# Optimization experiments

Measured on AMD Instinct MI355X. Metric: run time of the kernel, lower is better.

The kernel has to match this reference:

```python
import jax, jax.numpy as jnp
import numpy as np

C = 1000      # num_classes
U = 10        # proxies_per_class
D = 512       # feature_dim
B = 4096      # batch
ALPHA = 32.0
DELTA = 0.1


def _l2norm(x, axis=-1):
    return x / jnp.linalg.norm(x, axis=axis, keepdims=True).clip(1e-12)


def setup_inputs() -> dict:
    key = jax.random.key(0)
    k1, k2, k3 = jax.random.split(key, 3)
    features = jax.random.normal(k1, (B, D), dtype=jnp.float32)
    labels = jax.random.randint(k2, (B,), 0, C)
    # proxies are initialized to row-normalized gaussians (as in __init__)
    proxies = _l2norm(jax.random.normal(k3, (C * U, D), dtype=jnp.float32))
    return {"features": features, "labels": labels, "proxies": proxies}


def reference(features, labels, proxies):
    # proxy_class_ids: [C*U], class id of each proxy
    class_ids = jnp.repeat(jnp.arange(C), U)

    x = _l2norm(features)          # [B, D]
    p = _l2norm(proxies)           # [P, D], P = C*U
    sim = x @ p.T                  # [B, P]

    # ---- infer_logits, agg='soft', tau=1 ----
    s = sim.reshape(B, C, U)       # per-class proxy similarities
    w = jax.nn.softmax(s, axis=2)
    logits = jnp.sum(w * s, axis=2)  # [B, C], tau=1 so no extra scaling

    # ---- _compute_proxy_loss (Proxy-Anchor) ----
    sim_t = sim.T                                         # [P, B]
    pos_mask = labels[None, :] == class_ids[:, None]      # [P, B]
    neg_inf = jnp.finfo(jnp.float32).min
    z_pos = jnp.where(pos_mask, -ALPHA * (sim_t - DELTA), neg_inf)
    z_neg = jnp.where(pos_mask, neg_inf, ALPHA * (sim_t + DELTA))
    lse_pos = jax.nn.logsumexp(z_pos, axis=1)             # [P]
    lse_neg = jax.nn.logsumexp(z_neg, axis=1)             # [P]
    pos_term = jax.nn.softplus(lse_pos)
    neg_term = jax.nn.softplus(lse_neg)
    has_pos = pos_mask.any(axis=1)
    pos_loss = jnp.where(has_pos, pos_term, 0.0).sum() / jnp.maximum(
        has_pos.sum(), 1).astype(jnp.float32)
    neg_loss = neg_term.mean()
    proxy_loss = pos_loss + neg_loss

    return logits, proxy_loss
```

## Files before the change

### kernel.cpp

```cpp
#include <hip/hip_runtime.h>
#include <hip/hip_bf16.h>

#define C_CLS   1000
#define U_PX    10
#define D_DIM   512
#define B_BATCH 4096
#define P_PX    (C_CLS * U_PX)
#define ALPHA_F 32.0f
#define DELTA_F 0.1f

#define BM 128
#define BN 80
#define BK 64
#define SIMP 84

#define A_OFF   0
#define B_OFF   16384
#define SMEM_SZ 26624

#define ZERO_DBL (2 * P_PX + 4)
#define FIN_BLK  ((P_PX + 255) / 256)

typedef __attribute__((ext_vector_type(8))) short bf16x8;
typedef __attribute__((ext_vector_type(4))) float f32x4;

typedef __attribute__((address_space(1))) const void gv_t;
typedef __attribute__((address_space(3))) void lv_t;

__device__ __forceinline__ void gload_lds16(const void* g, void* lds) {
    __builtin_amdgcn_global_load_lds((gv_t*)g, (lv_t*)lds, 16, 0, 0);
}

__device__ __forceinline__ unsigned int f2bf(float f) {
    union { float f; unsigned u; } c; c.f = f;
    unsigned u = c.u;
    return (u + 0x7FFF + ((u >> 16) & 1)) >> 16;
}

__global__ __launch_bounds__(256) void norm_rows_kernel(const float* __restrict__ feat,
                                                        const float* __restrict__ prox,
                                                        unsigned int* __restrict__ xout,
                                                        unsigned int* __restrict__ pout,
                                                        double* __restrict__ zbase) {
    const int zidx = blockIdx.x * 256 + threadIdx.x;
    if (zidx < ZERO_DBL) zbase[zidx] = 0.0;

    const int wid  = threadIdx.x >> 6;
    const int lane = threadIdx.x & 63;
    int row = blockIdx.x * 4 + wid;
    const float* in;
    unsigned int* out;
    if (row < B_BATCH) { in = feat + (size_t)row * D_DIM;   out = xout + (size_t)row * (D_DIM / 2); }
    else { row -= B_BATCH; in = prox + (size_t)row * D_DIM; out = pout + (size_t)row * (D_DIM / 2); }
    const float4 v0 = reinterpret_cast<const float4*>(in)[lane * 2];
    const float4 v1 = reinterpret_cast<const float4*>(in)[lane * 2 + 1];
    float ss = v0.x*v0.x + v0.y*v0.y + v0.z*v0.z + v0.w*v0.w
             + v1.x*v1.x + v1.y*v1.y + v1.z*v1.z + v1.w*v1.w;
    #pragma unroll
    for (int off = 1; off < 64; off <<= 1) ss += __shfl_xor(ss, off, 64);
    const float inv = 1.0f / fmaxf(sqrtf(ss), 1e-12f);
    uint4 o;
    o.x = f2bf(v0.x * inv) | (f2bf(v0.y * inv) << 16);
    o.y = f2bf(v0.z * inv) | (f2bf(v0.w * inv) << 16);
    o.z = f2bf(v1.x * inv) | (f2bf(v1.y * inv) << 16);
    o.w = f2bf(v1.z * inv) | (f2bf(v1.w * inv) << 16);
    *reinterpret_cast<uint4*>(out + lane * 4) = o;
}

__global__ __launch_bounds__(256, 4) void fused_gemm_kernel(
    const unsigned short* __restrict__ xbf,
    const unsigned short* __restrict__ pbf,
    const int*            __restrict__ labels,
    float*                __restrict__ logits,
    double*               __restrict__ pos_sum,
    double*               __restrict__ neg_sum)
{
    __shared__ __align__(16) char smem[SMEM_SZ];
    __shared__ int lab_lds[BM];

    const int t    = threadIdx.x;
    const int m0   = blockIdx.x * BM;
    const int n0   = blockIdx.y * BN;
    const int wid  = t >> 6;
    const int lane = t & 63;
    const int l15  = lane & 15;
    const int kgrp = lane >> 4;

    if (t < BM) lab_lds[t] = labels[m0 + t];

    const int srow = lane >> 3;
    const int scol = (lane & 7) ^ srow;

    const int koff0 = ((kgrp    ) ^ (l15 & 7)) << 4;
    const int koff1 = ((kgrp + 4) ^ (l15 & 7)) << 4;

    f32x4 acc[2][5];
    #pragma unroll
    for (int m = 0; m < 2; ++m)
        #pragma unroll
        for (int n = 0; n < 5; ++n) acc[m][n] = (f32x4){0.f, 0.f, 0.f, 0.f};

    for (int ks = 0; ks < D_DIM / BK; ++ks) {
        const int kbase = ks * BK;
        #pragma unroll
        for (int c = wid; c < 16; c += 4)
            gload_lds16(xbf + (size_t)(m0 + c * 8 + srow) * D_DIM + kbase + scol * 8,
                        smem + A_OFF + c * 1024);
        for (int c = wid; c < 10; c += 4)
            gload_lds16(pbf + (size_t)(n0 + c * 8 + srow) * D_DIM + kbase + scol * 8,
                        smem + B_OFF + c * 1024);
        __syncthreads();
        __builtin_amdgcn_s_setprio(1);
        #pragma unroll
        for (int kk8 = 0; kk8 < 2; ++kk8) {
            const int koff = kk8 ? koff1 : koff0;
            bf16x8 b[5];
            #pragma unroll
            for (int n = 0; n < 5; ++n)
                b[n] = *reinterpret_cast<const bf16x8*>(smem + B_OFF + (n * 16 + l15) * 128 + koff);
            #pragma unroll
            for (int m = 0; m < 2; ++m) {
                const bf16x8 a = *reinterpret_cast<const bf16x8*>(
                    smem + A_OFF + (wid * 32 + m * 16 + l15) * 128 + koff);
                #pragma unroll
                for (int n = 0; n < 5; ++n)
                    acc[m][n] = __builtin_amdgcn_mfma_f32_16x16x32_bf16(a, b[n], acc[m][n], 0, 0, 0);
            }
        }
        __builtin_amdgcn_s_setprio(0);
        __syncthreads();
    }

    {
        int labv[8];
        #pragma unroll
        for (int m = 0; m < 2; ++m)
            #pragma unroll
            for (int r = 0; r < 4; ++r)
                labv[m * 4 + r] = lab_lds[wid * 32 + m * 16 + kgrp * 4 + r];
        #pragma unroll
        for (int n = 0; n < 5; ++n) {
            const int col = n * 16 + l15;
            const int cls = (n0 + col) / U_PX;
            float pos = 0.f, neg = 0.f;
            #pragma unroll
            for (int m = 0; m < 2; ++m)
                #pragma unroll
                for (int r = 0; r < 4; ++r) {
                    const float s = acc[m][n][r];
                    const bool isp = (labv[m * 4 + r] == cls);
                    const float e = __expf(isp ? (-ALPHA_F * (s - DELTA_F))
                                               : ( ALPHA_F * (s + DELTA_F)));
                    if (isp) pos += e; else neg += e;
                }
            pos += __shfl_xor(pos, 16, 64); pos += __shfl_xor(pos, 32, 64);
            neg += __shfl_xor(neg, 16, 64); neg += __shfl_xor(neg, 32, 64);
            if (lane < 16) {
                atomicAdd(&neg_sum[n0 + col], (double)neg);
                if (pos != 0.f) atomicAdd(&pos_sum[n0 + col], (double)pos);
            }
        }
    }

    float* simw = reinterpret_cast<float*>(smem) + wid * (16 * SIMP);
    #pragma unroll
    for (int m = 0; m < 2; ++m) {
        #pragma unroll
        for (int n = 0; n < 5; ++n)
            #pragma unroll
            for (int r = 0; r < 4; ++r)
                simw[(kgrp * 4 + r) * SIMP + n * 16 + l15] = acc[m][n][r];
        #pragma unroll
        for (int it = 0; it < 2; ++it) {
            const int j   = lane + it * 64;
            const int r   = j >> 3;
            const int c   = j & 7;
            const float* s = simw + r * SIMP + c * U_PX;
            float wsum = 0.f, wssum = 0.f;
            #pragma unroll
            for (int u = 0; u < U_PX; ++u) {
                const float sv = s[u];
                const float e = __expf(sv);
                wsum += e; wssum += e * sv;
            }
            logits[(size_t)(m0 + wid * 32 + m * 16 + r) * C_CLS + (n0 / U_PX + c)] = wssum / wsum;
        }
        __builtin_amdgcn_s_waitcnt(0);
    }
}

__global__ __launch_bounds__(256) void finalize_kernel(
    const double* __restrict__ pos_sum,
    const double* __restrict__ neg_sum,
    double*       __restrict__ accum,
    float*        __restrict__ out_loss)
{
    const int p = blockIdx.x * 256 + threadIdx.x;
    double pv = 0.0, nv = 0.0;
    int c = 0;
    if (p < P_PX) {
        nv = log1p(neg_sum[p]);
        const double ps = pos_sum[p];
        if (ps != 0.0) { pv = log1p(ps); c = 1; }
    }
    #pragma unroll
    for (int off = 1; off < 64; off <<= 1) {
        pv += __shfl_xor(pv, off, 64);
        nv += __shfl_xor(nv, off, 64);
        c  += __shfl_xor(c,  off, 64);
    }
    if ((threadIdx.x & 63) == 0) {
        atomicAdd(&accum[0], pv);
        atomicAdd(&accum[1], nv);
        atomicAdd((int*)(accum + 2), c);
    }
    __syncthreads();
    __threadfence();
    if (threadIdx.x == 0) {
        const unsigned prev = atomicAdd((unsigned*)(accum + 3), 1u);
        if (prev == FIN_BLK - 1) {
            const double a0 = atomicAdd(&accum[0], 0.0);
            const double a1 = atomicAdd(&accum[1], 0.0);
            const int   cnt = atomicAdd((int*)(accum + 2), 0);
            out_loss[0] = (float)(a0 / (double)max(cnt, 1) + a1 / (double)P_PX);
        }
    }
}

extern "C" void kernel_launch(void* const* d_in, const int* in_sizes, int n_in,
                              void* d_out, int out_size, void* d_ws, size_t ws_size,
                              hipStream_t stream) {
    const float* features = (const float*)d_in[0];
    const int*   labels   = (const int*)d_in[1];
    const float* proxies  = (const float*)d_in[2];
    float* out = (float*)d_out;

    char* ws = (char*)d_ws;
    unsigned short* xbf = (unsigned short*)ws;
    unsigned short* pbf = (unsigned short*)(ws + (size_t)B_BATCH * D_DIM * 2);
    double* pos_sum = (double*)(ws + (size_t)(B_BATCH + P_PX) * D_DIM * 2);
    double* neg_sum = pos_sum + P_PX;
    double* accum   = neg_sum + P_PX;

    norm_rows_kernel<<<(B_BATCH + P_PX) / 4, 256, 0, stream>>>(
        features, proxies, (unsigned int*)xbf, (unsigned int*)pbf, pos_sum);

    fused_gemm_kernel<<<dim3(B_BATCH / BM, P_PX / BN), 256, 0, stream>>>(
        xbf, pbf, labels, out, pos_sum, neg_sum);

    finalize_kernel<<<FIN_BLK, 256, 0, stream>>>(pos_sum, neg_sum, accum,
                                                 out + (size_t)B_BATCH * C_CLS);
}
```

Baseline: 93.96 us.

## Keep full A row-panel resident in LDS and loop persistently over proxy tiles

Each block now loads its whole 128x512 feature panel into LDS once (128KB) and loops over 16 proxy tiles in a persistent grid of 256 blocks, instead of reloading A per output tile. Proxy tiles are double-buffered so the next K slice is fetched while MFMAs run. The aim is to cut redundant global/L2 traffic for A and per-block launch/prologue costs. In exchange, the large LDS footprint limits occupancy to one block per CU, and the grid of 256 blocks may leave load-balance tails.

```diff
diff --git a/kernel.cpp b/kernel.cpp
--- a/kernel.cpp
+++ b/kernel.cpp
@@ -12,11 +12,14 @@
 #define BM 128
 #define BN 80
 #define BK 64
-#define SIMP 84
-
-#define A_OFF   0
-#define B_OFF   16384
-#define SMEM_SZ 26624
+#define NKS (D_DIM / BK)
+#define NNT (P_PX / BN)
+#define SIMP 80
+
+#define A_OFF    0
+#define B_OFF    131072
+#define B_STRIDE 10240
+#define SMEM_SZ  (131072 + 2 * B_STRIDE)
 
 #define ZERO_DBL (2 * P_PX + 4)
 #define FIN_BLK  ((P_PX + 255) / 256)
@@ -67,7 +70,7 @@
     *reinterpret_cast<uint4*>(out + lane * 4) = o;
 }
 
-__global__ __launch_bounds__(256, 4) void fused_gemm_kernel(
+__global__ __launch_bounds__(256) void fused_gemm_kernel(
     const unsigned short* __restrict__ xbf,
     const unsigned short* __restrict__ pbf,
     const int*            __restrict__ labels,
@@ -79,8 +82,10 @@
     __shared__ int lab_lds[BM];
 
     const int t    = threadIdx.x;
-    const int m0   = blockIdx.x * BM;
-    const int n0   = blockIdx.y * BN;
+    const int bx   = blockIdx.x;
+    const int mi   = bx >> 3;
+    const int nr   = bx & 7;
+    const int m0   = mi * BM;
     const int wid  = t >> 6;
     const int lane = t & 63;
     const int l15  = lane & 15;
@@ -88,105 +93,136 @@
 
     if (t < BM) lab_lds[t] = labels[m0 + t];
 
-    const int srow = lane >> 3;
-    const int scol = (lane & 7) ^ srow;
-
+    const int srow  = lane >> 3;
+    const int scolB = (lane & 7) ^ srow;
     const int koff0 = ((kgrp    ) ^ (l15 & 7)) << 4;
     const int koff1 = ((kgrp + 4) ^ (l15 & 7)) << 4;
 
+    for (int c = wid; c < BM; c += 4) {
+        const int gc = lane ^ (c & 7);
+        gload_lds16(xbf + (size_t)(m0 + c) * D_DIM + gc * 8,
+                    smem + A_OFF + c * 1024);
+    }
+    {
+        const int n0f = nr * BN;
+        for (int c = wid; c < 10; c += 4)
+            gload_lds16(pbf + (size_t)(n0f + c * 8 + srow) * D_DIM + scolB * 8,
+                        smem + B_OFF + c * 1024);
+    }
+    asm volatile("s_waitcnt vmcnt(0)\n\ts_barrier" ::: "memory");
+
     f32x4 acc[2][5];
-    #pragma unroll
-    for (int m = 0; m < 2; ++m)
-        #pragma unroll
-        for (int n = 0; n < 5; ++n) acc[m][n] = (f32x4){0.f, 0.f, 0.f, 0.f};
-
-    for (int ks = 0; ks < D_DIM / BK; ++ks) {
-        const int kbase = ks * BK;
-        #pragma unroll
-        for (int c = wid; c < 16; c += 4)
-            gload_lds16(xbf + (size_t)(m0 + c * 8 + srow) * D_DIM + kbase + scol * 8,
-                        smem + A_OFF + c * 1024);
-        for (int c = wid; c < 10; c += 4)
-            gload_lds16(pbf + (size_t)(n0 + c * 8 + srow) * D_DIM + kbase + scol * 8,
-                        smem + B_OFF + c * 1024);
-        __syncthreads();
-        __builtin_amdgcn_s_setprio(1);
-        #pragma unroll
-        for (int kk8 = 0; kk8 < 2; ++kk8) {
-            const int koff = kk8 ? koff1 : koff0;
-            bf16x8 b[5];
-            #pragma unroll
-            for (int n = 0; n < 5; ++n)
-                b[n] = *reinterpret_cast<const bf16x8*>(smem + B_OFF + (n * 16 + l15) * 128 + koff);
-            #pragma unroll
-            for (int m = 0; m < 2; ++m) {
-                const bf16x8 a = *reinterpret_cast<const bf16x8*>(
-                    smem + A_OFF + (wid * 32 + m * 16 + l15) * 128 + koff);
-                #pragma unroll
-                for (int n = 0; n < 5; ++n)
-                    acc[m][n] = __builtin_amdgcn_mfma_f32_16x16x32_bf16(a, b[n], acc[m][n], 0, 0, 0);
-            }
-        }
-        __builtin_amdgcn_s_setprio(0);
-        __syncthreads();
-    }
-
-    {
-        int labv[8];
+
+    #define STAGE_B(n0_, ks_, buf_)                                                     \
+        do {                                                                            \
+            for (int c_ = wid; c_ < 10; c_ += 4)                                        \
+                gload_lds16(pbf + (size_t)((n0_) + c_ * 8 + srow) * D_DIM               \
+                                + (ks_) * BK + scolB * 8,                               \
+                            smem + B_OFF + (buf_) * B_STRIDE + c_ * 1024);              \
+        } while (0)
+
+    for (int jt = nr; jt < NNT; jt += 8) {
+        const int n0 = jt * BN;
         #pragma unroll
         for (int m = 0; m < 2; ++m)
             #pragma unroll
-            for (int r = 0; r < 4; ++r)
-                labv[m * 4 + r] = lab_lds[wid * 32 + m * 16 + kgrp * 4 + r];
+            for (int n = 0; n < 5; ++n) acc[m][n] = (f32x4){0.f, 0.f, 0.f, 0.f};
+
+        for (int ks = 0; ks < NKS; ++ks) {
+            const int cur = ks & 1;
+            if (ks < NKS - 1) STAGE_B(n0, ks + 1, cur ^ 1);
+            __builtin_amdgcn_sched_barrier(0);
+            __builtin_amdgcn_s_setprio(1);
+            #pragma unroll
+            for (int kk8 = 0; kk8 < 2; ++kk8) {
+                const int koff = kk8 ? koff1 : koff0;
+                bf16x8 b[5];
+                #pragma unroll
+                for (int n = 0; n < 5; ++n)
+                    b[n] = *reinterpret_cast<const bf16x8*>(
+                        smem + B_OFF + cur * B_STRIDE + (n * 16 + l15) * 128 + koff);
+                const int kch = ks * 8 + kk8 * 4 + kgrp;
+                const int aoff = ((kch ^ (l15 & 7)) << 4);
+                #pragma unroll
+                for (int m = 0; m < 2; ++m) {
+                    const bf16x8 a = *reinterpret_cast<const bf16x8*>(
+                        smem + A_OFF + (wid * 32 + m * 16 + l15) * 1024 + aoff);
+                    #pragma unroll
+                    for (int n = 0; n < 5; ++n)
+                        acc[m][n] = __builtin_amdgcn_mfma_f32_16x16x32_bf16(
+                            a, b[n], acc[m][n], 0, 0, 0);
+                }
+            }
+            __builtin_amdgcn_s_setprio(0);
+            asm volatile("s_waitcnt lgkmcnt(0)" ::: "memory");
+            __builtin_amdgcn_sched_barrier(0);
+            asm volatile("s_waitcnt vmcnt(0)\n\ts_barrier" ::: "memory");
+        }
+
+        {
+            int labv[8];
+            #pragma unroll
+            for (int m = 0; m < 2; ++m)
+                #pragma unroll
+                for (int r = 0; r < 4; ++r)
+                    labv[m * 4 + r] = lab_lds[wid * 32 + m * 16 + kgrp * 4 + r];
+            #pragma unroll
+            for (int n = 0; n < 5; ++n) {
+                const int col = n * 16 + l15;
+                const int cls = (n0 + col) / U_PX;
+                float pos = 0.f, neg = 0.f;
+                #pragma unroll
+                for (int m = 0; m < 2; ++m)
+                    #pragma unroll
+                    for (int r = 0; r < 4; ++r) {
+                        const float s = acc[m][n][r];
+                        const bool isp = (labv[m * 4 + r] == cls);
+                        const float e = __expf(isp ? (-ALPHA_F * (s - DELTA_F))
+                                                   : ( ALPHA_F * (s + DELTA_F)));
+                        if (isp) pos += e; else neg += e;
+                    }
+                pos += __shfl_xor(pos, 16, 64); pos += __shfl_xor(pos, 32, 64);
+                neg += __shfl_xor(neg, 16, 64); neg += __shfl_xor(neg, 32, 64);
+                if (lane < 16) {
+                    atomicAdd(&neg_sum[n0 + col], (double)neg);
+                    if (pos != 0.f) atomicAdd(&pos_sum[n0 + col], (double)pos);
+                }
+            }
+        }
+
+        float* simw = reinterpret_cast<float*>(smem + B_OFF) + wid * (16 * SIMP);
         #pragma unroll
-        for (int n = 0; n < 5; ++n) {
-            const int col = n * 16 + l15;
-            const int cls = (n0 + col) / U_PX;
-            float pos = 0.f, neg = 0.f;
-            #pragma unroll
-            for (int m = 0; m < 2; ++m)
-                #pragma unroll
-                for (int r = 0; r < 4; ++r) {
-                    const float s = acc[m][n][r];
-                    const bool isp = (labv[m * 4 + r] == cls);
-                    const float e = __expf(isp ? (-ALPHA_F * (s - DELTA_F))
-                                               : ( ALPHA_F * (s + DELTA_F)));
-                    if (isp) pos += e; else neg += e;
+        for (int m = 0; m < 2; ++m) {
+            #pragma unroll
+            for (int n = 0; n < 5; ++n)
+                #pragma unroll
+                for (int r = 0; r < 4; ++r)
+                    simw[(kgrp * 4 + r) * SIMP + n * 16 + l15] = acc[m][n][r];
+            #pragma unroll
+            for (int it = 0; it < 2; ++it) {
+                const int j = lane + it * 64;
+                const int r = j >> 3;
+                const int c = j & 7;
+                const float* s = simw + r * SIMP + c * U_PX;
+                float wsum = 0.f, wssum = 0.f;
+                #pragma unroll
+                for (int u = 0; u < U_PX; ++u) {
+                    const float sv = s[u];
+                    const float e = __expf(sv);
+                    wsum += e; wssum += e * sv;
                 }
-            pos += __shfl_xor(pos, 16, 64); pos += __shfl_xor(pos, 32, 64);
-            neg += __shfl_xor(neg, 16, 64); neg += __shfl_xor(neg, 32, 64);
-            if (lane < 16) {
-                atomicAdd(&neg_sum[n0 + col], (double)neg);
-                if (pos != 0.f) atomicAdd(&pos_sum[n0 + col], (double)pos);
+                logits[(size_t)(m0 + wid * 32 + m * 16 + r) * C_CLS + (jt * 8 + c)] = wssum / wsum;
             }
-        }
-    }
-
-    float* simw = reinterpret_cast<float*>(smem) + wid * (16 * SIMP);
-    #pragma unroll
-    for (int m = 0; m < 2; ++m) {
-        #pragma unroll
-        for (int n = 0; n < 5; ++n)
-            #pragma unroll
-            for (int r = 0; r < 4; ++r)
-                simw[(kgrp * 4 + r) * SIMP + n * 16 + l15] = acc[m][n][r];
-        #pragma unroll
-        for (int it = 0; it < 2; ++it) {
-            const int j   = lane + it * 64;
-            const int r   = j >> 3;
-            const int c   = j & 7;
-            const float* s = simw + r * SIMP + c * U_PX;
-            float wsum = 0.f, wssum = 0.f;
-            #pragma unroll
-            for (int u = 0; u < U_PX; ++u) {
-                const float sv = s[u];
-                const float e = __expf(sv);
-                wsum += e; wssum += e * sv;
-            }
-            logits[(size_t)(m0 + wid * 32 + m * 16 + r) * C_CLS + (n0 / U_PX + c)] = wssum / wsum;
-        }
-        __builtin_amdgcn_s_waitcnt(0);
-    }
+            __builtin_amdgcn_s_waitcnt(0);
+        }
+
+        __builtin_amdgcn_s_barrier();
+        if (jt + 8 < NNT) {
+            STAGE_B((jt + 8) * BN, 0, 0);
+            asm volatile("s_waitcnt vmcnt(0)\n\ts_barrier" ::: "memory");
+        }
+    }
+    #undef STAGE_B
 }
 
 __global__ __launch_bounds__(256) void finalize_kernel(
@@ -245,7 +281,7 @@
     norm_rows_kernel<<<(B_BATCH + P_PX) / 4, 256, 0, stream>>>(
         features, proxies, (unsigned int*)xbf, (unsigned int*)pbf, pos_sum);
 
-    fused_gemm_kernel<<<dim3(B_BATCH / BM, P_PX / BN), 256, 0, stream>>>(
+    fused_gemm_kernel<<<(B_BATCH / BM) * 8, 256, 0, stream>>>(
         xbf, pbf, labels, out, pos_sum, neg_sum);
 
     finalize_kernel<<<FIN_BLK, 256, 0, stream>>>(pos_sum, neg_sum, accum,
```

After: 182.4 us. +94.1%, slower.
